# Performance work log

Measured on AMD Instinct MI355X. Metric: run time of the kernel, lower is better.

Reference implementation:

```python
import jax, jax.numpy as jnp
import numpy as np
from jax import lax

C = 16        # class_nums
START = 14    # tag_to_idx['<START>']
STOP = 15     # tag_to_idx['<STOP>']
NEG = -10000.0
B, T, V, E, H = 64, 512, 50000, 512, 1024
HD = H // 2   # per-direction hidden size


def setup_inputs() -> dict:
    key = jax.random.key(0)
    ks = jax.random.split(key, 16)
    s = 0.05
    inp = {}
    inp["sentence"] = jax.random.randint(ks[0], (B, T), 0, V)
    inp["embedding"] = jax.random.normal(ks[1], (V, E), jnp.float32) * 0.1
    # LSTM params, torch layout: [4*HD, Din] with gate order i,f,g,o; leading dim 2 = (fwd, bwd)
    inp["w_ih_l0"] = jax.random.normal(ks[2], (2, 4 * HD, E), jnp.float32) * s
    inp["w_hh_l0"] = jax.random.normal(ks[3], (2, 4 * HD, HD), jnp.float32) * s
    inp["b_ih_l0"] = jax.random.normal(ks[4], (2, 4 * HD), jnp.float32) * s
    inp["b_hh_l0"] = jax.random.normal(ks[5], (2, 4 * HD), jnp.float32) * s
    inp["w_ih_l1"] = jax.random.normal(ks[6], (2, 4 * HD, H), jnp.float32) * s
    inp["w_hh_l1"] = jax.random.normal(ks[7], (2, 4 * HD, HD), jnp.float32) * s
    inp["b_ih_l1"] = jax.random.normal(ks[8], (2, 4 * HD), jnp.float32) * s
    inp["b_hh_l1"] = jax.random.normal(ks[9], (2, 4 * HD), jnp.float32) * s
    inp["lin_w"] = jax.random.normal(ks[10], (C, H), jnp.float32) * s
    inp["lin_b"] = jax.random.normal(ks[11], (C,), jnp.float32) * s
    tr = jax.random.normal(ks[12], (C, C), jnp.float32)
    inp["transitions"] = tr.at[START, :].set(NEG).at[:, STOP].set(NEG)
    # init_hidden(): random (h0, c0), shape [2*num_layers, B, HD]
    inp["h0"] = jax.random.normal(ks[13], (4, B, HD), jnp.float32)
    inp["c0"] = jax.random.normal(ks[14], (4, B, HD), jnp.float32)
    return inp


def _lstm_dir(x, w_ih, w_hh, b_ih, b_hh, h0, c0, reverse):
    # x: [T, B, Din] -> hs: [T, B, HD]
    def step(carry, xt):
        h, c = carry
        g = xt @ w_ih.T + h @ w_hh.T + b_ih + b_hh  # [B, 4*HD]
        i, f, gc, o = jnp.split(g, 4, axis=-1)       # torch gate order: i, f, g, o
        c = jax.nn.sigmoid(f) * c + jax.nn.sigmoid(i) * jnp.tanh(gc)
        h = jax.nn.sigmoid(o) * jnp.tanh(c)
        return (h, c), h
    _, hs = lax.scan(step, (h0, c0), x, reverse=reverse)
    return hs


def _features(sentence, embedding, w_ih_l0, w_hh_l0, b_ih_l0, b_hh_l0,
              w_ih_l1, w_hh_l1, b_ih_l1, b_hh_l1, lin_w, lin_b, h0, c0):
    x = embedding[sentence].transpose(1, 0, 2)  # [T, B, E]
    # layer 0 (bidirectional)
    hf = _lstm_dir(x, w_ih_l0[0], w_hh_l0[0], b_ih_l0[0], b_hh_l0[0], h0[0], c0[0], False)
    hb = _lstm_dir(x, w_ih_l0[1], w_hh_l0[1], b_ih_l0[1], b_hh_l0[1], h0[1], c0[1], True)
    x = jnp.concatenate([hf, hb], axis=-1)      # [T, B, H]
    # layer 1 (bidirectional)
    hf = _lstm_dir(x, w_ih_l1[0], w_hh_l1[0], b_ih_l1[0], b_hh_l1[0], h0[2], c0[2], False)
    hb = _lstm_dir(x, w_ih_l1[1], w_hh_l1[1], b_ih_l1[1], b_hh_l1[1], h0[3], c0[3], True)
    x = jnp.concatenate([hf, hb], axis=-1)      # [T, B, H]
    feats = x @ lin_w.T + lin_b                 # [T, B, C]
    return feats.transpose(1, 0, 2)             # [B, T, C]


def _viterbi(feats, transitions):
    # feats: [T, C]. Vectorized over the tag dim; scan over time.
    init = jnp.full((C,), NEG, feats.dtype).at[START].set(0.0)

    def step(fv, feat_t):
        scores = fv[None, :] + transitions      # [next_tag, prev_tag]
        bp = jnp.argmax(scores, axis=1)
        return jnp.max(scores, axis=1) + feat_t, bp

    fv, bps = lax.scan(step, init, feats)       # bps: [T, C]
    terminal = fv + transitions[STOP]
    best = jnp.argmax(terminal)

    def back(tag, bp_t):
        return bp_t[tag], tag

    _, path = lax.scan(back, best, bps, reverse=True)  # [T]
    return terminal[best], path


def reference(sentence, embedding, w_ih_l0, w_hh_l0, b_ih_l0, b_hh_l0,
              w_ih_l1, w_hh_l1, b_ih_l1, b_hh_l1, lin_w, lin_b,
              transitions, h0, c0):
    feats = _features(sentence, embedding, w_ih_l0, w_hh_l0, b_ih_l0, b_hh_l0,
                      w_ih_l1, w_hh_l1, b_ih_l1, b_hh_l1, lin_w, lin_b, h0, c0)
    scores, paths = jax.vmap(_viterbi, in_axes=(0, None))(feats, transitions)
    return scores, paths
```

## Files before the change

kernel.cpp:

```cpp
#include <hip/hip_runtime.h>
#include <stdint.h>

constexpr int kB  = 64;
constexpr int kT  = 512;
constexpr int kHD = 512;
constexpr int kC  = 16;
constexpr int kL  = 32;
constexpr int kSTART = 14;
constexpr int kSTOP  = 15;
#define NEGV (-10000.0f)

typedef __bf16 bf16x8 __attribute__((ext_vector_type(8)));
typedef float  f32x4  __attribute__((ext_vector_type(4)));

union U16x8 { uint4 u; bf16x8 v; };

__device__ __forceinline__ unsigned short f2bf(float f) {
    union { float f; unsigned int u; } x; x.f = f;
    unsigned int u = x.u;
    u += 0x7fffu + ((u >> 16) & 1u);
    return (unsigned short)(u >> 16);
}
__device__ __forceinline__ float bf2f(unsigned int hbits) {
    union { unsigned int u; float f; } x; x.u = hbits << 16;
    return x.f;
}

typedef __attribute__((address_space(1))) const unsigned int GASU;
typedef __attribute__((address_space(3))) unsigned int LASU;
__device__ __forceinline__ void ld_lds16(const unsigned short* g, unsigned short* l) {
    __builtin_amdgcn_global_load_lds((GASU*)g, (LASU*)l, 16, 0, 0);
}

__global__ void k_castWx(const float* __restrict__ src, unsigned short* __restrict__ dst, int K) {
    int np = blockIdx.x;
    int dd = np >> 11, r = np & 2047;
    int g = r & 3, cj = r >> 2;
    const float* s = src + ((size_t)(dd * 2048 + g * 512 + cj)) * K;
    unsigned short* d = dst + (size_t)np * K;
    for (int e = threadIdx.x * 8; e < K; e += 128 * 8) {
        float4 a = *(const float4*)(s + e);
        float4 b = *(const float4*)(s + e + 4);
        ushort4 lo, hi;
        lo.x = f2bf(a.x); lo.y = f2bf(a.y); lo.z = f2bf(a.z); lo.w = f2bf(a.w);
        hi.x = f2bf(b.x); hi.y = f2bf(b.y); hi.z = f2bf(b.z); hi.w = f2bf(b.w);
        *(ushort4*)(d + e) = lo; *(ushort4*)(d + e + 4) = hi;
    }
}

__global__ void k_embed(const int* __restrict__ sent, const float* __restrict__ emb,
                        unsigned short* __restrict__ X0) {
    int row = blockIdx.x;
    int t = row >> 6, b = row & 63;
    int v = sent[b * kT + t];
    const float4* src = (const float4*)(emb + (size_t)v * 512);
    float4 f = src[threadIdx.x];
    ushort4 o;
    o.x = f2bf(f.x); o.y = f2bf(f.y); o.z = f2bf(f.z); o.w = f2bf(f.w);
    ((ushort4*)(X0 + (size_t)row * 512))[threadIdx.x] = o;
}

__global__ void k_init(const float* __restrict__ h0, const float* __restrict__ c0,
                       const float* __restrict__ bih0, const float* __restrict__ bhh0,
                       const float* __restrict__ bih1, const float* __restrict__ bhh1,
                       const float* __restrict__ lw,
                       unsigned short* __restrict__ hcur, float* __restrict__ ccur,
                       float* __restrict__ biascat0, float* __restrict__ biascat1,
                       unsigned int* __restrict__ flags, unsigned short* __restrict__ lwb) {
    int i = blockIdx.x * blockDim.x + threadIdx.x;
    const int NS = 4 * kB * kHD;
    if (i < NS) {
        int l = i >> 16;
        int rem = i & 65535;
        hcur[(size_t)l * 131072 + rem] = f2bf(h0[i]);
        ccur[i] = c0[i];
    } else if (i < NS + 8192) {
        int j2 = i - NS;
        int l = j2 >> 12;
        int n = j2 & 4095;
        int dd = n >> 11, r = n & 2047;
        int g = r >> 9, cj = r & 511;
        float v = l ? (bih1[n] + bhh1[n]) : (bih0[n] + bhh0[n]);
        int np = dd * 2048 + cj * 4 + g;
        (l ? biascat1 : biascat0)[np] = v;
    } else if (i < NS + 8192 + 2048) {
        flags[i - NS - 8192] = 0u;
    } else if (i < NS + 8192 + 2048 + 16384) {
        int idx = i - NS - 8192 - 2048;
        lwb[idx] = f2bf(lw[idx]);
    }
}

__launch_bounds__(256, 2)
__global__ void k_gemm(const unsigned short* __restrict__ A,
                       const unsigned short* __restrict__ Bm,
                       const float* __restrict__ bias,
                       unsigned short* __restrict__ Cm,
                       int K, int afwd, int abwd) {
    const int nb = blockIdx.x & 31;
    const int mb = blockIdx.x >> 5;
    const int m0w = mb << 7;
    const int arow0 = (m0w < 2048) ? (afwd + m0w) : (abwd + (m0w - 2048));
    const int n0 = nb << 7;
    const int tid = threadIdx.x;
    const int lane = tid & 63;
    const int wave = tid >> 6;
    const int wm = wave >> 1, wn = wave & 1;
    const int l16 = lane & 15, quad = lane >> 4;
    __shared__ unsigned short As[128 * 32];
    __shared__ unsigned short Bs[128 * 32];
    const int srw = wave * 32 + (lane >> 2);
    const int sc  = lane & 3;
    unsigned short* AsW0 = As + wave * 1024;
    unsigned short* AsW1 = As + wave * 1024 + 512;
    unsigned short* BsW0 = Bs + wave * 1024;
    unsigned short* BsW1 = Bs + wave * 1024 + 512;

    f32x4 acc[4][4];
    #pragma unroll
    for (int i = 0; i < 4; ++i)
        #pragma unroll
        for (int jj = 0; jj < 4; ++jj) acc[i][jj] = (f32x4){0,0,0,0};

    const int kiters = K >> 5;
    for (int kk = 0; kk < kiters; ++kk) {
        __syncthreads();
        ld_lds16(A  + (size_t)(arow0 + srw)      * K + kk * 32 + sc * 8, AsW0);
        ld_lds16(A  + (size_t)(arow0 + srw + 16) * K + kk * 32 + sc * 8, AsW1);
        ld_lds16(Bm + (size_t)(n0 + srw)         * K + kk * 32 + sc * 8, BsW0);
        ld_lds16(Bm + (size_t)(n0 + srw + 16)    * K + kk * 32 + sc * 8, BsW1);
        __syncthreads();
        U16x8 af[4], bf[4];
        #pragma unroll
        for (int i = 0; i < 4; ++i) {
            af[i].u = *(const uint4*)(As + (wm * 64 + i * 16 + l16) * 32 + quad * 8);
            bf[i].u = *(const uint4*)(Bs + (wn * 64 + i * 16 + l16) * 32 + quad * 8);
        }
        #pragma unroll
        for (int i = 0; i < 4; ++i)
            #pragma unroll
            for (int jj = 0; jj < 4; ++jj)
                acc[i][jj] = __builtin_amdgcn_mfma_f32_16x16x32_bf16(af[i].v, bf[jj].v, acc[i][jj], 0, 0, 0);
    }
    #pragma unroll
    for (int jj = 0; jj < 4; ++jj) {
        int n = n0 + wn * 64 + jj * 16 + l16;
        float bv = bias[n];
        #pragma unroll
        for (int i = 0; i < 4; ++i) {
            int mrow = m0w + wm * 64 + i * 16 + quad * 4;
            #pragma unroll
            for (int rr = 0; rr < 4; ++rr)
                Cm[(size_t)(mrow + rr) * 4096 + n] = f2bf(acc[i][jj][rr] + bv);
        }
    }
}

__launch_bounds__(512, 1)
__global__ void k_fused(const unsigned short* __restrict__ Wh,
                        const unsigned short* __restrict__ Gx,
                        unsigned short* __restrict__ hcur,
                        float* __restrict__ cc,
                        unsigned short* __restrict__ hs,
                        unsigned short* __restrict__ S,
                        unsigned int* __restrict__ flags,
                        int s0, int split,
                        const unsigned short* __restrict__ Ag,
                        const unsigned short* __restrict__ Wxg,
                        const float* __restrict__ biasg,
                        unsigned short* __restrict__ Gxout,
                        int Kg, int gfwd, int gbwd, int do_gemm) {
    __shared__ __align__(16) char smem[52736];
    const int tid = threadIdx.x;

    if (blockIdx.x < 64) {
        unsigned short* zbuf   = (unsigned short*)smem;
        float*          gs     = (float*)(smem + 33280);
        unsigned short* hstash = (unsigned short*)(smem + 50688);
        const int blk = blockIdx.x;
        const int d  = blk >> 5;
        const int bh = (blk >> 4) & 1;
        const int wc = blk & 15;
        const int wave = tid >> 6;
        const int lane = tid & 63;
        const int l16 = lane & 15;
        const int quad = lane >> 4;

        uint4 wreg[16];
        {
            const unsigned short* wrow =
                Wh + ((size_t)d * 2048 + wc * 128 + wave * 16 + l16) * 512 + quad * 8;
            #pragma unroll
            for (int kk = 0; kk < 16; ++kk) wreg[kk] = *(const uint4*)(wrow + kk * 32);
        }
        const int m16 = tid >> 5;
        const int j   = tid & 31;
        float cst[2];
        #pragma unroll
        for (int mt = 0; mt < 2; ++mt)
            cst[mt] = cc[((size_t)d * 64 + bh * 32 + mt * 16 + m16) * 512 + wc * 32 + j];

        unsigned int* flg = flags + (d * 2 + bh) * 256;

        for (int sl = 0; sl < kL; ++sl) {
            const int s = s0 + sl;
            const int t = d ? (kT - 1 - s) : s;
            ushort4 gx4[2];
            #pragma unroll
            for (int mt = 0; mt < 2; ++mt) {
                int b = bh * 32 + mt * 16 + m16;
                int grow = d ? (2048 + (kL - 1 - sl) * 64 + b) : (sl * 64 + b);
                gx4[mt] = *(const ushort4*)(Gx + (size_t)grow * 4096 + d * 2048 + (wc * 32 + j) * 4);
            }
            if (sl > 0) {
                if (wave == 0 && lane < 16) {
                    unsigned tgt = (unsigned)s;
                    while (__hip_atomic_load(flg + lane * 16, __ATOMIC_RELAXED,
                                             __HIP_MEMORY_SCOPE_AGENT) < tgt)
                        __builtin_amdgcn_s_sleep(1);
                }
                __syncthreads();
            }
            {
                const unsigned long long* hread = (const unsigned long long*)
                    (hcur + ((size_t)((s & 1) * 2 + d) * 64 + bh * 32) * 512);
                #pragma unroll
                for (int k = 0; k < 8; ++k) {
                    int idx = tid + k * 512;
                    int r = idx >> 7, c8 = idx & 127;
                    unsigned long long v = __hip_atomic_load(hread + r * 128 + c8,
                                                             __ATOMIC_RELAXED,
                                                             __HIP_MEMORY_SCOPE_AGENT);
                    *(unsigned long long*)(zbuf + r * 520 + c8 * 4) = v;
                }
            }
            __syncthreads();
            f32x4 acc[2];
            acc[0] = (f32x4){0, 0, 0, 0};
            acc[1] = (f32x4){0, 0, 0, 0};
            #pragma unroll
            for (int kk = 0; kk < 16; ++kk) {
                U16x8 b; b.u = wreg[kk];
                #pragma unroll
                for (int mt = 0; mt < 2; ++mt) {
                    U16x8 a; a.u = *(const uint4*)(zbuf + (mt * 16 + l16) * 520 + kk * 32 + quad * 8);
                    acc[mt] = __builtin_amdgcn_mfma_f32_16x16x32_bf16(a.v, b.v, acc[mt], 0, 0, 0);
                }
            }
            #pragma unroll
            for (int mt = 0; mt < 2; ++mt)
                #pragma unroll
                for (int rr = 0; rr < 4; ++rr)
                    gs[((mt * 8 + wave) * 16 + quad * 4 + rr) * 17 + l16] = acc[mt][rr];
            __syncthreads();
            #pragma unroll
            for (int mt = 0; mt < 2; ++mt) {
                float gi = gs[((mt * 8 + (j >> 2)) * 16 + m16) * 17 + (j & 3) * 4 + 0] + bf2f(gx4[mt].x);
                float gf = gs[((mt * 8 + (j >> 2)) * 16 + m16) * 17 + (j & 3) * 4 + 1] + bf2f(gx4[mt].y);
                float gg = gs[((mt * 8 + (j >> 2)) * 16 + m16) * 17 + (j & 3) * 4 + 2] + bf2f(gx4[mt].z);
                float go = gs[((mt * 8 + (j >> 2)) * 16 + m16) * 17 + (j & 3) * 4 + 3] + bf2f(gx4[mt].w);
                float si = 1.f / (1.f + __expf(-gi));
                float sf = 1.f / (1.f + __expf(-gf));
                float so = 1.f / (1.f + __expf(-go));
                float tg = tanhf(gg);
                float cn = sf * cst[mt] + si * tg;
                cst[mt] = cn;
                float hn = so * tanhf(cn);
                hstash[(mt * 16 + m16) * 32 + j] = f2bf(hn);
            }
            __syncthreads();
            if (tid < 256) {
                int r = tid >> 3, u = tid & 7;
                unsigned long long val = *(const unsigned long long*)(hstash + r * 32 + u * 4);
                unsigned long long* hwrite = (unsigned long long*)
                    (hcur + ((size_t)(((s + 1) & 1) * 2 + d) * 64 + bh * 32) * 512);
                __hip_atomic_store(hwrite + r * 128 + wc * 8 + u, val,
                                   __ATOMIC_RELAXED, __HIP_MEMORY_SCOPE_AGENT);
                int b = bh * 32 + r;
                bool toS = split && (d ? (t >= 256) : (t < 256));
                if (toS)
                    *(unsigned long long*)(S + ((size_t)t * 64 + b) * 512 + wc * 32 + u * 4) = val;
                else
                    *(unsigned long long*)(hs + ((size_t)t * 64 + b) * 1024 + (size_t)d * 512 + wc * 32 + u * 4) = val;
            }
            __syncthreads();
            if (sl + 1 < kL && tid == 0)
                __hip_atomic_store(flg + wc * 16, (unsigned)(s + 1),
                                   __ATOMIC_RELAXED, __HIP_MEMORY_SCOPE_AGENT);
        }
        #pragma unroll
        for (int mt = 0; mt < 2; ++mt)
            cc[((size_t)d * 64 + bh * 32 + mt * 16 + m16) * 512 + wc * 32 + j] = cst[mt];
    } else {
        if (!do_gemm) return;
        const int gw = blockIdx.x - 64;
        const int half = tid >> 8;
        const int tid2 = tid & 255;
        const int w4 = tid2 >> 6;
        const int lane = tid2 & 63;
        const int l16 = lane & 15, quad = lane >> 4;
        unsigned short* As = (unsigned short*)(smem + half * 16384);
        unsigned short* Bs = (unsigned short*)(smem + half * 16384 + 8192);
        const int srw = w4 * 32 + (lane >> 2);
        const int sc  = lane & 3;
        const int wm = w4 >> 1, wn = w4 & 1;
        unsigned short* AsW0 = As + w4 * 1024;
        unsigned short* AsW1 = As + w4 * 1024 + 512;
        unsigned short* BsW0 = Bs + w4 * 1024;
        unsigned short* BsW1 = Bs + w4 * 1024 + 512;
        const int kiters = Kg >> 5;

        for (int pp = gw; pp < 512; pp += 192) {
            const int mb = pp >> 4;
            const int nb = ((pp & 15) << 1) + half;
            const int m0w = mb << 7;
            const int arow0 = (m0w < 2048) ? (gfwd + m0w) : (gbwd + (m0w - 2048));
            const int n0 = nb << 7;
            f32x4 acc[4][4];
            #pragma unroll
            for (int i = 0; i < 4; ++i)
                #pragma unroll
                for (int jj = 0; jj < 4; ++jj) acc[i][jj] = (f32x4){0,0,0,0};
            for (int kk = 0; kk < kiters; ++kk) {
                __syncthreads();
                ld_lds16(Ag  + (size_t)(arow0 + srw)      * Kg + kk * 32 + sc * 8, AsW0);
                ld_lds16(Ag  + (size_t)(arow0 + srw + 16) * Kg + kk * 32 + sc * 8, AsW1);
                ld_lds16(Wxg + (size_t)(n0 + srw)         * Kg + kk * 32 + sc * 8, BsW0);
                ld_lds16(Wxg + (size_t)(n0 + srw + 16)    * Kg + kk * 32 + sc * 8, BsW1);
                __syncthreads();
                U16x8 af[4], bf[4];
                #pragma unroll
                for (int i = 0; i < 4; ++i) {
                    af[i].u = *(const uint4*)(As + (wm * 64 + i * 16 + l16) * 32 + quad * 8);
                    bf[i].u = *(const uint4*)(Bs + (wn * 64 + i * 16 + l16) * 32 + quad * 8);
                }
                #pragma unroll
                for (int i = 0; i < 4; ++i)
                    #pragma unroll
                    for (int jj = 0; jj < 4; ++jj)
                        acc[i][jj] = __builtin_amdgcn_mfma_f32_16x16x32_bf16(af[i].v, bf[jj].v, acc[i][jj], 0, 0, 0);
            }
            #pragma unroll
            for (int jj = 0; jj < 4; ++jj) {
                int n = n0 + wn * 64 + jj * 16 + l16;
                float bv = biasg[n];
                #pragma unroll
                for (int i = 0; i < 4; ++i) {
                    int mrow = m0w + wm * 64 + i * 16 + quad * 4;
                    #pragma unroll
                    for (int rr = 0; rr < 4; ++rr)
                        Gxout[(size_t)(mrow + rr) * 4096 + n] = f2bf(acc[i][jj][rr] + bv);
                }
            }
        }
    }
}

__global__ void k_linear(const unsigned short* __restrict__ hs1,
                         const unsigned short* __restrict__ S,
                         const unsigned short* __restrict__ lwb,
                         const float* __restrict__ lb,
                         float* __restrict__ feats) {
    const int t = blockIdx.x;
    const int tid = threadIdx.x;
    const int wave = tid >> 6;
    const int lane = tid & 63;
    const int l16 = lane & 15, quad = lane >> 4;
    __shared__ unsigned short lws[16 * 1032];
    {
        #pragma unroll
        for (int i = 0; i < 8; ++i) {
            int idx = tid + i * 256;
            int n = idx >> 7, c = idx & 127;
            *(uint4*)(lws + n * 1032 + c * 8) = *(const uint4*)(lwb + n * 1024 + c * 8);
        }
    }
    __syncthreads();
    const int brow = wave * 16 + l16;
    f32x4 acc = {0, 0, 0, 0};
    #pragma unroll
    for (int kk = 0; kk < 32; ++kk) {
        int k0 = kk * 32 + quad * 8;
        const unsigned short* p;
        if (kk < 16)
            p = (t < 256) ? S   + ((size_t)t * 64 + brow) * 512  + k0
                          : hs1 + ((size_t)t * 64 + brow) * 1024 + k0;
        else
            p = (t >= 256) ? S   + ((size_t)t * 64 + brow) * 512  + (k0 - 512)
                           : hs1 + ((size_t)t * 64 + brow) * 1024 + k0;
        U16x8 a; a.u = *(const uint4*)p;
        U16x8 b; b.u = *(const uint4*)(lws + l16 * 1032 + k0);
        acc = __builtin_amdgcn_mfma_f32_16x16x32_bf16(a.v, b.v, acc, 0, 0, 0);
    }
    float bv = lb[l16];
    #pragma unroll
    for (int rr = 0; rr < 4; ++rr) {
        int b = wave * 16 + quad * 4 + rr;
        feats[(size_t)b * (kT * kC) + t * kC + l16] = acc[rr] + bv;
    }
}

__global__ void k_viterbi(const float* __restrict__ feats, const float* __restrict__ trans,
                          float* __restrict__ out) {
    int b = blockIdx.x;
    int lane = threadIdx.x;
    __shared__ unsigned char bp[kT * kC];
    __shared__ float fv[2][kC];
    __shared__ float tbuf[kC];
    float trow[16];
    float tstop = 0.f;
    if (lane < 16) {
        #pragma unroll
        for (int p = 0; p < 16; ++p) trow[p] = trans[lane * 16 + p];
        tstop = trans[kSTOP * 16 + lane];
        fv[0][lane] = (lane == kSTART) ? 0.f : NEGV;
    }
    __syncthreads();
    const float* fb = feats + (size_t)b * (kT * kC);
    for (int t = 0; t < kT; ++t) {
        if (lane < 16) {
            float m = -3.4e38f; int arg = 0;
            #pragma unroll
            for (int p = 0; p < 16; ++p) {
                float v = fv[t & 1][p] + trow[p];
                if (v > m) { m = v; arg = p; }
            }
            bp[t * 16 + lane] = (unsigned char)arg;
            fv[(t + 1) & 1][lane] = m + fb[t * 16 + lane];
        }
        __syncthreads();
    }
    if (lane < 16) tbuf[lane] = fv[kT & 1][lane] + tstop;
    __syncthreads();
    if (lane == 0) {
        float bm = tbuf[0]; int best = 0;
        #pragma unroll
        for (int p = 1; p < 16; ++p) if (tbuf[p] > bm) { bm = tbuf[p]; best = p; }
        out[b] = bm;
        float* path = out + kB + (size_t)b * kT;
        int tag = best;
        for (int t = kT - 1; t >= 0; --t) {
            path[t] = (float)tag;
            tag = bp[t * 16 + tag];
        }
    }
}

extern "C" void kernel_launch(void* const* d_in, const int* in_sizes, int n_in,
                              void* d_out, int out_size, void* d_ws, size_t ws_size,
                              hipStream_t stream) {
    const int*   sent = (const int*)d_in[0];
    const float* emb  = (const float*)d_in[1];
    const float* wih0 = (const float*)d_in[2];
    const float* whh0 = (const float*)d_in[3];
    const float* bih0 = (const float*)d_in[4];
    const float* bhh0 = (const float*)d_in[5];
    const float* wih1 = (const float*)d_in[6];
    const float* whh1 = (const float*)d_in[7];
    const float* bih1 = (const float*)d_in[8];
    const float* bhh1 = (const float*)d_in[9];
    const float* lw   = (const float*)d_in[10];
    const float* lb   = (const float*)d_in[11];
    const float* tr   = (const float*)d_in[12];
    const float* h0   = (const float*)d_in[13];
    const float* c0   = (const float*)d_in[14];
    float* out = (float*)d_out;

    char* ws = (char*)d_ws;
    size_t off = 0;
    auto alloc = [&](size_t bytes) -> void* {
        void* p = ws + off; off += (bytes + 255) & ~(size_t)255; return p;
    };
    unsigned short* X0    = (unsigned short*)alloc((size_t)kT * kB * 512 * 2);
    unsigned short* Wx0   = (unsigned short*)alloc((size_t)4096 * 512 * 2);
    unsigned short* S     = (unsigned short*)X0;
    unsigned short* Wh0   = (unsigned short*)alloc((size_t)4096 * 512 * 2);
    unsigned short* Wx1   = (unsigned short*)alloc((size_t)4096 * 1024 * 2);
    unsigned short* Wh1   = (unsigned short*)alloc((size_t)4096 * 512 * 2);
    float*          biascat0 = (float*)alloc(4096 * 4);
    float*          biascat1 = (float*)alloc(4096 * 4);
    unsigned short* HS    = (unsigned short*)alloc((size_t)kT * kB * 1024 * 2);
    unsigned short* hcur  = (unsigned short*)alloc((size_t)2 * 2 * 2 * kB * kHD * 2);
    float*          ccur  = (float*)alloc((size_t)4 * kB * kHD * 4);
    float*          feats = (float*)alloc((size_t)kB * kT * kC * 4);
    unsigned int*   flags = (unsigned int*)alloc(2048 * 4);
    unsigned short* lwb   = (unsigned short*)alloc(16384 * 2);
    unsigned short* Gx0   = (unsigned short*)alloc((size_t)4096 * 4096 * 2);
    unsigned short* Gx1   = (unsigned short*)alloc((size_t)4096 * 4096 * 2);
    unsigned short* GxB[2] = {Gx0, Gx1};

    k_castWx<<<4096, 128, 0, stream>>>(wih0, Wx0, 512);
    k_castWx<<<4096, 128, 0, stream>>>(whh0, Wh0, 512);
    k_castWx<<<4096, 128, 0, stream>>>(wih1, Wx1, 1024);
    k_castWx<<<4096, 128, 0, stream>>>(whh1, Wh1, 512);
    k_init<<<(4 * kB * kHD + 8192 + 2048 + 16384 + 255) / 256, 256, 0, stream>>>(
        h0, c0, bih0, bhh0, bih1, bhh1, lw, hcur, ccur, biascat0, biascat1, flags, lwb);
    k_embed<<<kT * kB, 128, 0, stream>>>(sent, emb, X0);

    unsigned short* hcur1 = hcur + (size_t)131072;
    float*          ccur1 = ccur + (size_t)65536;

    k_gemm<<<1024, 256, 0, stream>>>(X0, Wx0, biascat0, Gx0, 512, 0, (kT - kL) * 64);
    for (int ch = 0; ch < 16; ++ch) {
        int s0n = (ch + 1) * kL;
        k_fused<<<256, 512, 0, stream>>>(Wh0, GxB[ch & 1], hcur, ccur, HS, S, flags, ch * kL, 0,
                                         X0, Wx0, biascat0, GxB[(ch + 1) & 1], 512,
                                         s0n * 64, (kT - kL - s0n) * 64, ch < 15);
    }
    k_gemm<<<1024, 256, 0, stream>>>(HS, Wx1, biascat1, Gx0, 1024, 0, (kT - kL) * 64);
    for (int ch = 0; ch < 16; ++ch) {
        int s0n = (ch + 1) * kL;
        k_fused<<<256, 512, 0, stream>>>(Wh1, GxB[ch & 1], hcur1, ccur1, HS, S, flags + 1024, ch * kL, 1,
                                         HS, Wx1, biascat1, GxB[(ch + 1) & 1], 1024,
                                         s0n * 64, (kT - kL - s0n) * 64, ch < 15);
    }

    k_linear<<<kT, 256, 0, stream>>>(HS, S, lwb, lb, feats);
    k_viterbi<<<kB, 64, 0, stream>>>(feats, tr, out);
}
```

Baseline: 5.441 ms.

## Make LSTM gate epilogue wave-local and move hidden stores after flag publish

Each wave now keeps the gate columns its own MFMA tiles produced and runs the sigmoid/tanh cell update for those 4 hidden units itself. It stages through a per-wave LDS slice guarded by s_waitcnt instead of block-wide barriers. Every wave polls the step flags directly, which drops the barrier that followed polling. The hs/S output stores move after the flag publish so they sit off the recurrent critical path. The aim is to cut barriers and latency on each serial timestep. The cost is redundant flag polling in all waves and more reliance on manual LDS wait ordering.

```diff
diff --git a/kernel.cpp b/kernel.cpp
--- a/kernel.cpp
+++ b/kernel.cpp
@@ -175,8 +175,8 @@
 
     if (blockIdx.x < 64) {
         unsigned short* zbuf   = (unsigned short*)smem;
-        float*          gs     = (float*)(smem + 33280);
-        unsigned short* hstash = (unsigned short*)(smem + 50688);
+        float*          gsAll  = (float*)(smem + 33280);
+        unsigned short* hstA   = (unsigned short*)(smem + 50688);
         const int blk = blockIdx.x;
         const int d  = blk >> 5;
         const int bh = (blk >> 4) & 1;
@@ -185,6 +185,11 @@
         const int lane = tid & 63;
         const int l16 = lane & 15;
         const int quad = lane >> 4;
+        const int r4 = lane >> 2;
+        const int u  = lane & 3;
+        const int col = wc * 32 + wave * 4 + u;
+        float* gw = gsAll + wave * 544;
+        unsigned short* hw = hstA + wave * 128;
 
         uint4 wreg[16];
         {
@@ -193,12 +198,10 @@
             #pragma unroll
             for (int kk = 0; kk < 16; ++kk) wreg[kk] = *(const uint4*)(wrow + kk * 32);
         }
-        const int m16 = tid >> 5;
-        const int j   = tid & 31;
         float cst[2];
         #pragma unroll
         for (int mt = 0; mt < 2; ++mt)
-            cst[mt] = cc[((size_t)d * 64 + bh * 32 + mt * 16 + m16) * 512 + wc * 32 + j];
+            cst[mt] = cc[((size_t)d * 64 + bh * 32 + mt * 16 + r4) * 512 + col];
 
         unsigned int* flg = flags + (d * 2 + bh) * 256;
 
@@ -208,18 +211,15 @@
             ushort4 gx4[2];
             #pragma unroll
             for (int mt = 0; mt < 2; ++mt) {
-                int b = bh * 32 + mt * 16 + m16;
+                int b = bh * 32 + mt * 16 + r4;
                 int grow = d ? (2048 + (kL - 1 - sl) * 64 + b) : (sl * 64 + b);
-                gx4[mt] = *(const ushort4*)(Gx + (size_t)grow * 4096 + d * 2048 + (wc * 32 + j) * 4);
-            }
-            if (sl > 0) {
-                if (wave == 0 && lane < 16) {
-                    unsigned tgt = (unsigned)s;
-                    while (__hip_atomic_load(flg + lane * 16, __ATOMIC_RELAXED,
-                                             __HIP_MEMORY_SCOPE_AGENT) < tgt)
-                        __builtin_amdgcn_s_sleep(1);
-                }
-                __syncthreads();
+                gx4[mt] = *(const ushort4*)(Gx + (size_t)grow * 4096 + d * 2048 + col * 4);
+            }
+            if (sl > 0 && lane < 16) {
+                unsigned tgt = (unsigned)s;
+                while (__hip_atomic_load(flg + lane * 16, __ATOMIC_RELAXED,
+                                         __HIP_MEMORY_SCOPE_AGENT) < tgt)
+                    __builtin_amdgcn_s_sleep(1);
             }
             {
                 const unsigned long long* hread = (const unsigned long long*)
@@ -251,14 +251,16 @@
             for (int mt = 0; mt < 2; ++mt)
                 #pragma unroll
                 for (int rr = 0; rr < 4; ++rr)
-                    gs[((mt * 8 + wave) * 16 + quad * 4 + rr) * 17 + l16] = acc[mt][rr];
-            __syncthreads();
+                    gw[mt * 272 + (quad * 4 + rr) * 17 + l16] = acc[mt][rr];
+            asm volatile("s_waitcnt lgkmcnt(0)" ::: "memory");
+            __builtin_amdgcn_sched_barrier(0);
             #pragma unroll
             for (int mt = 0; mt < 2; ++mt) {
-                float gi = gs[((mt * 8 + (j >> 2)) * 16 + m16) * 17 + (j & 3) * 4 + 0] + bf2f(gx4[mt].x);
-                float gf = gs[((mt * 8 + (j >> 2)) * 16 + m16) * 17 + (j & 3) * 4 + 1] + bf2f(gx4[mt].y);
-                float gg = gs[((mt * 8 + (j >> 2)) * 16 + m16) * 17 + (j & 3) * 4 + 2] + bf2f(gx4[mt].z);
-                float go = gs[((mt * 8 + (j >> 2)) * 16 + m16) * 17 + (j & 3) * 4 + 3] + bf2f(gx4[mt].w);
+                const float* gb = gw + mt * 272 + r4 * 17 + u * 4;
+                float gi = gb[0] + bf2f(gx4[mt].x);
+                float gf = gb[1] + bf2f(gx4[mt].y);
+                float gg = gb[2] + bf2f(gx4[mt].z);
+                float go = gb[3] + bf2f(gx4[mt].w);
                 float si = 1.f / (1.f + __expf(-gi));
                 float sf = 1.f / (1.f + __expf(-gf));
                 float so = 1.f / (1.f + __expf(-go));
@@ -266,31 +268,34 @@
                 float cn = sf * cst[mt] + si * tg;
                 cst[mt] = cn;
                 float hn = so * tanhf(cn);
-                hstash[(mt * 16 + m16) * 32 + j] = f2bf(hn);
-            }
-            __syncthreads();
-            if (tid < 256) {
-                int r = tid >> 3, u = tid & 7;
-                unsigned long long val = *(const unsigned long long*)(hstash + r * 32 + u * 4);
+                hw[(mt * 16 + r4) * 4 + u] = f2bf(hn);
+            }
+            asm volatile("s_waitcnt lgkmcnt(0)" ::: "memory");
+            __builtin_amdgcn_sched_barrier(0);
+            unsigned long long hval = 0ull;
+            if (lane < 32) {
+                hval = *(const unsigned long long*)(hw + lane * 4);
                 unsigned long long* hwrite = (unsigned long long*)
                     (hcur + ((size_t)(((s + 1) & 1) * 2 + d) * 64 + bh * 32) * 512);
-                __hip_atomic_store(hwrite + r * 128 + wc * 8 + u, val,
+                __hip_atomic_store(hwrite + lane * 128 + wc * 8 + wave, hval,
                                    __ATOMIC_RELAXED, __HIP_MEMORY_SCOPE_AGENT);
-                int b = bh * 32 + r;
-                bool toS = split && (d ? (t >= 256) : (t < 256));
-                if (toS)
-                    *(unsigned long long*)(S + ((size_t)t * 64 + b) * 512 + wc * 32 + u * 4) = val;
-                else
-                    *(unsigned long long*)(hs + ((size_t)t * 64 + b) * 1024 + (size_t)d * 512 + wc * 32 + u * 4) = val;
             }
             __syncthreads();
             if (sl + 1 < kL && tid == 0)
                 __hip_atomic_store(flg + wc * 16, (unsigned)(s + 1),
                                    __ATOMIC_RELAXED, __HIP_MEMORY_SCOPE_AGENT);
+            if (lane < 32) {
+                int b = bh * 32 + lane;
+                bool toS = split && (d ? (t >= 256) : (t < 256));
+                if (toS)
+                    *(unsigned long long*)(S + ((size_t)t * 64 + b) * 512 + wc * 32 + wave * 4) = hval;
+                else
+                    *(unsigned long long*)(hs + ((size_t)t * 64 + b) * 1024 + (size_t)d * 512 + wc * 32 + wave * 4) = hval;
+            }
         }
         #pragma unroll
         for (int mt = 0; mt < 2; ++mt)
-            cc[((size_t)d * 64 + bh * 32 + mt * 16 + m16) * 512 + wc * 32 + j] = cst[mt];
+            cc[((size_t)d * 64 + bh * 32 + mt * 16 + r4) * 512 + col] = cst[mt];
     } else {
         if (!do_gemm) return;
         const int gw = blockIdx.x - 64;
```

Measured after the change: 5.680 ms. 4.4% more time.
